# Optimization experiments

Measured on AMD Instinct MI355X. Metric: run time of the kernel, lower is better.

Reference implementation:

```python
import jax, jax.numpy as jnp
import numpy as np

# Config (matches init_kwargs)
B, S = 2, 2048            # 2 packed sequences of 2048 tokens (prefill)
HQ, HK, D = 32, 8, 128    # GQA: 32 query heads, 8 kv heads
G = HQ // HK              # group size 4
WINDOW = 1024             # sliding window
THETA = 10000.0


def setup_inputs() -> dict:
    key = jax.random.key(0)
    kq, kk, kv = jax.random.split(key, 3)
    n_tokens = B * S
    query = jax.random.normal(kq, (n_tokens, HQ * D), dtype=jnp.float32)
    key_t = jax.random.normal(kk, (n_tokens, HK * D), dtype=jnp.float32)
    value = jax.random.normal(kv, (n_tokens, HK * D), dtype=jnp.float32)
    # per-sequence positions restart at 0 for each packed sequence
    positions = jnp.tile(jnp.arange(S, dtype=jnp.int32), B)
    return {"query": query, "key": key_t, "value": value, "positions": positions}


def _rope(x, positions):
    # x: [B, S, H, D]; rotate-half (NeoX) RoPE
    half = D // 2
    inv_freq = 1.0 / (THETA ** (jnp.arange(0, half, dtype=jnp.float32) / half))
    ang = positions.astype(jnp.float32)[:, None] * inv_freq[None, :]   # [B*S, D/2]
    cos = jnp.cos(ang).reshape(B, S, 1, half)
    sin = jnp.sin(ang).reshape(B, S, 1, half)
    x1, x2 = x[..., :half], x[..., half:]
    return jnp.concatenate([x1 * cos - x2 * sin, x2 * cos + x1 * sin], axis=-1)


def reference(query, key, value, positions):
    q = query.reshape(B, S, HQ, D)
    k = key.reshape(B, S, HK, D)
    v = value.reshape(B, S, HK, D)
    q = _rope(q, positions)
    k = _rope(k, positions)
    # GQA: split q heads into [HK, G]
    qg = q.reshape(B, S, HK, G, D)
    scale = 1.0 / jnp.sqrt(jnp.float32(D))
    # scores: [B, HK, G, Sq, Skv]
    scores = jnp.einsum('bqhgd,bshd->bhgqs', qg, k) * scale
    i = jnp.arange(S)[:, None]
    j = jnp.arange(S)[None, :]
    # causal + sliding window: j <= i and i - j < WINDOW
    mask = (j <= i) & ((i - j) < WINDOW)
    scores = jnp.where(mask[None, None, None], scores, jnp.float32(-1e30))
    attn = jax.nn.softmax(scores, axis=-1)
    out = jnp.einsum('bhgqs,bshd->bqhgd', attn, v)   # [B, Sq, HK, G, D]
    return out.reshape(B * S, HQ * D)
```

## Files before the change

### kernel.cpp

```cpp
#include <hip/hip_runtime.h>
#include <stdint.h>

#define NB 2
#define NS 2048
#define NHK 8
#define ND 128
#define NWIN 1024

using bf16x8 = __bf16 __attribute__((ext_vector_type(8)));
using f32x4  = float  __attribute__((ext_vector_type(4)));
using f32x8  = float  __attribute__((ext_vector_type(8)));
using u16x8  = unsigned short __attribute__((ext_vector_type(8)));
using u32x4  = unsigned int   __attribute__((ext_vector_type(4)));

#define L2_10K (13.287712379549449f / 64.0f)
#define MASKV (-3.0e38f)

static __device__ __forceinline__ float ex2(float x) {
  return __builtin_amdgcn_exp2f(x);
}

static __device__ __forceinline__ unsigned short f2bf(float x) {
  unsigned int u = __builtin_bit_cast(unsigned int, x);
  u += 0x7FFFu + ((u >> 16) & 1u);
  return (unsigned short)(u >> 16);
}

static __device__ __forceinline__ unsigned int cvtpk(float lo, float hi) {
  unsigned int r;
  asm("v_cvt_pk_bf16_f32 %0, %1, %2" : "=v"(r) : "v"(lo), "v"(hi));
  return r;
}

static __device__ __forceinline__ void gll16(const void* g, void* l) {
  __builtin_amdgcn_global_load_lds(
      (const __attribute__((address_space(1))) void*)g,
      (__attribute__((address_space(3))) void*)l, 16, 0, 0);
}

#define ROR(x, N) __builtin_bit_cast(float, __builtin_amdgcn_mov_dpp( \
    __builtin_bit_cast(int, (x)), 0x120 + (N), 0xF, 0xF, false))

__global__ __launch_bounds__(64) void build_tab(float* __restrict__ tab) {
  const int p = blockIdx.x, f = threadIdx.x;
  float s, c;
  __sincosf((float)p * ex2(-(float)f * L2_10K), &s, &c);
  tab[(size_t)p * 128 + f] = c;
  tab[(size_t)p * 128 + 64 + f] = s;
}

__global__ __launch_bounds__(256) void prepass(
    const float* __restrict__ kin, const float* __restrict__ vin,
    const int* __restrict__ pos, const float* __restrict__ tab,
    unsigned short* __restrict__ kimg, unsigned int* __restrict__ vimg) {
  const int bid = blockIdx.x;
  const int ti = bid & 63, gidx = bid >> 6;
  const int hk = gidx & 7, b = gidx >> 3;
  const int t = threadIdx.x;

  unsigned short* kout = kimg + (size_t)bid * 4096;
#pragma unroll
  for (int uu = 0; uu < 2; ++uu) {
    const int u = t * 2 + uu;
    const int j = u >> 4;
    const int d0 = ((u & 15) << 3) ^ ((j & 7) << 3);
    const int tok = (b << 11) + (ti << 5) + j;
    const float* kp = kin + (size_t)tok * (NHK * ND) + hk * ND;
    f32x8 a = *(const f32x8*)(kp + d0);
    f32x8 p = *(const f32x8*)(kp + (d0 ^ 64));
    const float* tr = tab + (size_t)(pos[tok] & 2047) * 128 + (d0 & 63);
    f32x8 c8 = *(const f32x8*)tr;
    f32x8 s8 = *(const f32x8*)(tr + 64);
    u16x8 o;
#pragma unroll
    for (int i = 0; i < 8; ++i) {
      float val = (d0 < 64) ? (a[i] * c8[i] - p[i] * s8[i])
                            : (a[i] * c8[i] + p[i] * s8[i]);
      o[i] = f2bf(val);
    }
    *(u16x8*)(kout + (size_t)u * 8) = o;
  }

  unsigned int* vout = vimg + (size_t)bid * 2048;
  {
    const int d = t >> 1;
    const int jp0 = (t & 1) << 3;
    const float* vp = vin + (size_t)((b << 11) + (ti << 5)) * (NHK * ND) + hk * ND + d;
    unsigned int o[8];
#pragma unroll
    for (int i = 0; i < 8; ++i)
      o[i] = cvtpk(vp[(size_t)(jp0 + i) * (NHK * ND)],
                   vp[(size_t)(jp0 + i + 16) * (NHK * ND)]);
    u32x4 w0 = {o[0], o[1], o[2], o[3]};
    u32x4 w1 = {o[4], o[5], o[6], o[7]};
    *(u32x4*)(vout + d * 16 + jp0) = w0;
    *(u32x4*)(vout + d * 16 + jp0 + 4) = w1;
  }
}

template <bool PRE>
__global__ __launch_bounds__(256, 2) void attn_fwd(
    const float* __restrict__ qin, const float* __restrict__ kin,
    const float* __restrict__ vin, const int* __restrict__ pos,
    const char* __restrict__ kimg, const char* __restrict__ vimg,
    float* __restrict__ out) {
  __shared__ __align__(16) char Kb[2][8192];
  __shared__ __align__(16) char Vb[2][8192];
  __shared__ __align__(16) unsigned int Pw[4][32 * 20];

  const int B = blockIdx.x;
  const int group = (B & 7) + ((B >> 9) << 3);
  const int qt = 63 - ((B >> 3) & 63);
  const int hk = group & 7, b = group >> 3;

  const int tid = threadIdx.x;
  const int w = tid >> 6, lane = tid & 63, h = lane >> 4, ln = lane & 15;
  const int g = w;
  const int q0b = qt << 5;
  int lo = q0b - (NWIN - 1);
  if (lo < 0) lo = 0;
  lo &= ~31;
  const int ti0 = lo >> 5;
  const int nt = (q0b >> 5) - ti0 + 1;

  const size_t gbase = (size_t)group * 64 * 8192;
  const char* kg = PRE ? kimg + gbase + (size_t)(w * 128 + lane) * 16 : nullptr;
  const char* vg = PRE ? vimg + gbase + (size_t)(w * 128 + lane) * 16 : nullptr;

  auto stage = [&](int cur, int ti) {
    if constexpr (PRE) {
      const char* ks = kg + (size_t)ti * 8192;
      const char* vs = vg + (size_t)ti * 8192;
      char* kd = &Kb[cur][w * 2048];
      char* vd = &Vb[cur][w * 2048];
      gll16(ks, kd);
      gll16(ks + 1024, kd + 1024);
      gll16(vs, vd);
      gll16(vs + 1024, vd + 1024);
    } else {
      const int j = tid >> 3;
      const int du = (tid & 7) << 4;
      const int tok = (b << 11) + (ti << 5) + j;
      const float* kp = kin + (size_t)tok * (NHK * ND) + hk * ND;
      const float pj = (float)pos[tok];
#pragma unroll
      for (int gq = 0; gq < 2; ++gq) {
        const int dd = du + gq * 8;
        f32x8 a = *(const f32x8*)(kp + dd);
        f32x8 p = *(const f32x8*)(kp + (dd ^ 64));
        u16x8 o;
#pragma unroll
        for (int i = 0; i < 8; ++i) {
          float s, c;
          __sincosf(pj * ex2(-(float)((dd & 63) + i) * L2_10K), &s, &c);
          float val = (dd < 64) ? (a[i] * c - p[i] * s) : (a[i] * c + p[i] * s);
          o[i] = f2bf(val);
        }
        *(u16x8*)(&Kb[cur][((j << 8) + (dd << 1)) ^ ((j & 7) << 4)]) = o;
      }
      const int d = tid >> 1;
      const int jp0 = (tid & 1) << 3;
      const float* vp = vin + (size_t)((b << 11) + (ti << 5)) * (NHK * ND) + hk * ND + d;
      unsigned int o[8];
#pragma unroll
      for (int i = 0; i < 8; ++i)
        o[i] = cvtpk(vp[(size_t)(jp0 + i) * (NHK * ND)],
                     vp[(size_t)(jp0 + i + 16) * (NHK * ND)]);
      unsigned int* vb32 = (unsigned int*)Vb[cur];
      u32x4 w0 = {o[0], o[1], o[2], o[3]};
      u32x4 w1 = {o[4], o[5], o[6], o[7]};
      *(u32x4*)(vb32 + d * 16 + jp0) = w0;
      *(u32x4*)(vb32 + d * 16 + jp0 + 4) = w1;
    }
  };

  stage(0, ti0);

  const float QSC = 0.08838834764831845f * 1.4426950408889634f;
  bf16x8 qfr[2][4];
#pragma unroll
  for (int hf = 0; hf < 2; ++hf) {
    const int qrow = q0b + hf * 16 + ln;
    const size_t tokq = (size_t)(b << 11) + qrow;
    const float* qp = qin + tokq * 4096 + (hk * 4 + g) * 128;
    const float posq = (float)pos[tokq];
    const int r0 = h << 3;
    const int r1 = 32 + (h << 3);
    f32x8 a0 = *(const f32x8*)(qp + r0);
    f32x8 a1 = *(const f32x8*)(qp + r1);
    f32x8 a2 = *(const f32x8*)(qp + r0 + 64);
    f32x8 a3 = *(const f32x8*)(qp + r1 + 64);
    u16x8 u0, u1, u2, u3;
#pragma unroll
    for (int i = 0; i < 8; ++i) {
      float c0, s0, c1, s1;
      __sincosf(posq * ex2(-(float)(r0 + i) * L2_10K), &s0, &c0);
      __sincosf(posq * ex2(-(float)(r1 + i) * L2_10K), &s1, &c1);
      u0[i] = f2bf((a0[i] * c0 - a2[i] * s0) * QSC);
      u1[i] = f2bf((a1[i] * c1 - a3[i] * s1) * QSC);
      u2[i] = f2bf((a2[i] * c0 + a0[i] * s0) * QSC);
      u3[i] = f2bf((a3[i] * c1 + a1[i] * s1) * QSC);
    }
    qfr[hf][0] = __builtin_bit_cast(bf16x8, u0);
    qfr[hf][1] = __builtin_bit_cast(bf16x8, u1);
    qfr[hf][2] = __builtin_bit_cast(bf16x8, u2);
    qfr[hf][3] = __builtin_bit_cast(bf16x8, u3);
  }

  f32x4 Oc[2][8] = {};
  float m[2][4] = {{-1e30f, -1e30f, -1e30f, -1e30f},
                   {-1e30f, -1e30f, -1e30f, -1e30f}};
  float lsum[2][4] = {};
  unsigned int* pw = Pw[w];
  const int sw = (ln & 7) << 4;

  for (int t = 0; t < nt; ++t) {
    const int cur = t & 1;
    asm volatile("s_waitcnt vmcnt(0)" ::: "memory");
    __syncthreads();
    if (t + 1 < nt) stage(cur ^ 1, ti0 + t + 1);

    const int j0 = (ti0 + t) << 5;
    const char* KB = Kb[cur];

    f32x4 sS[2][2] = {};
    __builtin_amdgcn_s_setprio(1);
#pragma unroll
    for (int c = 0; c < 4; ++c) {
      const bf16x8 k0 = *(const bf16x8*)(
          KB + (((ln << 8) + (c << 6) + (h << 4)) ^ sw));
      const bf16x8 k1 = *(const bf16x8*)(
          KB + ((((16 + ln) << 8) + (c << 6) + (h << 4)) ^ sw));
      sS[0][0] = __builtin_amdgcn_mfma_f32_16x16x32_bf16(qfr[0][c], k0, sS[0][0], 0, 0, 0);
      sS[0][1] = __builtin_amdgcn_mfma_f32_16x16x32_bf16(qfr[0][c], k1, sS[0][1], 0, 0, 0);
      sS[1][0] = __builtin_amdgcn_mfma_f32_16x16x32_bf16(qfr[1][c], k0, sS[1][0], 0, 0, 0);
      sS[1][1] = __builtin_amdgcn_mfma_f32_16x16x32_bf16(qfr[1][c], k1, sS[1][1], 0, 0, 0);
    }
    __builtin_amdgcn_s_setprio(0);

    if ((j0 >= q0b) || (j0 < q0b - 992)) {
#pragma unroll
      for (int hf = 0; hf < 2; ++hf)
#pragma unroll
        for (int r = 0; r < 4; ++r) {
          const int irow = q0b + hf * 16 + (h << 2) + r;
          const int jc0 = j0 + ln, jc1 = jc0 + 16;
          if (!(jc0 <= irow && irow - jc0 < NWIN)) sS[hf][0][r] = MASKV;
          if (!(jc1 <= irow && irow - jc1 < NWIN)) sS[hf][1][r] = MASKV;
        }
    }

    float ov = MASKV;
    float tmax[2][4];
#pragma unroll
    for (int hf = 0; hf < 2; ++hf)
#pragma unroll
      for (int r = 0; r < 4; ++r) {
        tmax[hf][r] = fmaxf(sS[hf][0][r], sS[hf][1][r]);
        ov = fmaxf(ov, tmax[hf][r] - m[hf][r]);
      }
    if (__any(ov > 8.0f)) {
#pragma unroll
      for (int hf = 0; hf < 2; ++hf)
#pragma unroll
        for (int r = 0; r < 4; ++r) {
          float tm = tmax[hf][r];
          tm = fmaxf(tm, ROR(tm, 1));
          tm = fmaxf(tm, ROR(tm, 2));
          tm = fmaxf(tm, ROR(tm, 4));
          tm = fmaxf(tm, ROR(tm, 8));
          const float mn = fmaxf(m[hf][r], tm);
          const float co = ex2(m[hf][r] - mn);
          m[hf][r] = mn;
          lsum[hf][r] *= co;
#pragma unroll
          for (int db = 0; db < 8; ++db) Oc[hf][db][r] *= co;
        }
    }
#pragma unroll
    for (int hf = 0; hf < 2; ++hf)
#pragma unroll
      for (int r = 0; r < 4; ++r) {
        const float e0 = ex2(sS[hf][0][r] - m[hf][r]);
        const float e1 = ex2(sS[hf][1][r] - m[hf][r]);
        lsum[hf][r] += e0 + e1;
        pw[(hf * 16 + (h << 2) + r) * 20 + ln] = cvtpk(e0, e1);
      }

    asm volatile("s_waitcnt lgkmcnt(0)" ::: "memory");
    const bf16x8 pa0 = *(const bf16x8*)(pw + (ln * 20 + (h << 2)));
    const bf16x8 pa1 = *(const bf16x8*)(pw + ((16 + ln) * 20 + (h << 2)));
    const unsigned int* VB = (const unsigned int*)Vb[cur];
    __builtin_amdgcn_s_setprio(1);
#pragma unroll
    for (int db = 0; db < 8; ++db) {
      const bf16x8 vv = *(const bf16x8*)(VB + ((((db << 4) + ln) << 4) + (h << 2)));
      Oc[0][db] = __builtin_amdgcn_mfma_f32_16x16x32_bf16(pa0, vv, Oc[0][db], 0, 0, 0);
      Oc[1][db] = __builtin_amdgcn_mfma_f32_16x16x32_bf16(pa1, vv, Oc[1][db], 0, 0, 0);
    }
    __builtin_amdgcn_s_setprio(0);
  }

#pragma unroll
  for (int hf = 0; hf < 2; ++hf)
#pragma unroll
    for (int r = 0; r < 4; ++r) {
      float rs = lsum[hf][r];
      rs += ROR(rs, 1);
      rs += ROR(rs, 2);
      rs += ROR(rs, 4);
      rs += ROR(rs, 8);
      const float rl = 1.0f / rs;
      const int irow = q0b + hf * 16 + (h << 2) + r;
      float* op = out + ((size_t)(b << 11) + irow) * 4096 + (hk * 4 + g) * 128 + ln;
#pragma unroll
      for (int db = 0; db < 8; ++db) op[db * 16] = Oc[hf][db][r] * rl;
    }
}

extern "C" void kernel_launch(void* const* d_in, const int* in_sizes, int n_in,
                              void* d_out, int out_size, void* d_ws, size_t ws_size,
                              hipStream_t stream) {
  const float* q = (const float*)d_in[0];
  const float* k = (const float*)d_in[1];
  const float* v = (const float*)d_in[2];
  const int* pos = (const int*)d_in[3];
  float* out = (float*)d_out;

  const size_t TAB = (size_t)2048 * 128 * 4;
  const size_t KIMG = (size_t)16 * 64 * 8192;
  const size_t need = TAB + 2 * KIMG;

  if (ws_size >= need) {
    float* tab = (float*)d_ws;
    char* kimg = (char*)d_ws + TAB;
    char* vimg = kimg + KIMG;
    build_tab<<<2048, 64, 0, stream>>>(tab);
    prepass<<<1024, 256, 0, stream>>>(k, v, pos, tab,
                                      (unsigned short*)kimg, (unsigned int*)vimg);
    attn_fwd<true><<<1024, 256, 0, stream>>>(q, k, v, pos, kimg, vimg, out);
  } else {
    attn_fwd<false><<<1024, 256, 0, stream>>>(q, k, v, pos, nullptr, nullptr, out);
  }
}
```

Baseline: 112.4 us.

## Compute transposed scores so P feeds PV MFMA via permlane swaps, dropping LDS

Swaps the MFMA operands so the score tile comes out transposed (keys per lane-group, queries per lane). The softmax probabilities can then be repacked into the PV A-operand with v_permlane32/16_swap instead of a round trip through LDS. Row max and sum now need cross-lane shuffles. The V image layout changes to match the new operand layout, the per-wave P scratch buffer is removed, and occupancy hint rises to 3 blocks per CU. Risks: extra shuffles in the rescale path, and register pressure under the tighter launch bound.

```diff
diff --git a/kernel.cpp b/kernel.cpp
--- a/kernel.cpp
+++ b/kernel.cpp
@@ -9,6 +9,7 @@
 
 using bf16x8 = __bf16 __attribute__((ext_vector_type(8)));
 using f32x4  = float  __attribute__((ext_vector_type(4)));
+using f32x2  = float  __attribute__((ext_vector_type(2)));
 using f32x8  = float  __attribute__((ext_vector_type(8)));
 using u16x8  = unsigned short __attribute__((ext_vector_type(8)));
 using u32x4  = unsigned int   __attribute__((ext_vector_type(4)));
@@ -37,9 +38,6 @@
       (const __attribute__((address_space(1))) void*)g,
       (__attribute__((address_space(3))) void*)l, 16, 0, 0);
 }
-
-#define ROR(x, N) __builtin_bit_cast(float, __builtin_amdgcn_mov_dpp( \
-    __builtin_bit_cast(int, (x)), 0x120 + (N), 0xF, 0xF, false))
 
 __global__ __launch_bounds__(64) void build_tab(float* __restrict__ tab) {
   const int p = blockIdx.x, f = threadIdx.x;
@@ -52,7 +50,7 @@
 __global__ __launch_bounds__(256) void prepass(
     const float* __restrict__ kin, const float* __restrict__ vin,
     const int* __restrict__ pos, const float* __restrict__ tab,
-    unsigned short* __restrict__ kimg, unsigned int* __restrict__ vimg) {
+    unsigned short* __restrict__ kimg, unsigned short* __restrict__ vimg) {
   const int bid = blockIdx.x;
   const int ti = bid & 63, gidx = bid >> 6;
   const int hk = gidx & 7, b = gidx >> 3;
@@ -81,32 +79,33 @@
     *(u16x8*)(kout + (size_t)u * 8) = o;
   }
 
-  unsigned int* vout = vimg + (size_t)bid * 2048;
+  unsigned short* vout = vimg + (size_t)bid * 4096;
   {
-    const int d = t >> 1;
-    const int jp0 = (t & 1) << 3;
-    const float* vp = vin + (size_t)((b << 11) + (ti << 5)) * (NHK * ND) + hk * ND + d;
-    unsigned int o[8];
-#pragma unroll
-    for (int i = 0; i < 8; ++i)
-      o[i] = cvtpk(vp[(size_t)(jp0 + i) * (NHK * ND)],
-                   vp[(size_t)(jp0 + i + 16) * (NHK * ND)]);
-    u32x4 w0 = {o[0], o[1], o[2], o[3]};
-    u32x4 w1 = {o[4], o[5], o[6], o[7]};
-    *(u32x4*)(vout + d * 16 + jp0) = w0;
-    *(u32x4*)(vout + d * 16 + jp0 + 4) = w1;
+    const int d0 = (t >> 2) << 1;
+    const int kp4 = t & 3;
+    const int tok0 = (b << 11) + (ti << 5) + (kp4 << 3);
+    const float* vp = vin + (size_t)tok0 * (NHK * ND) + hk * ND + d0;
+    u16x8 lo, hi;
+#pragma unroll
+    for (int i = 0; i < 8; ++i) {
+      f32x2 r = *(const f32x2*)(vp + (size_t)i * (NHK * ND));
+      lo[i] = f2bf(r[0]);
+      hi[i] = f2bf(r[1]);
+    }
+    const int sub = kp4 ^ ((d0 >> 1) & 3);
+    *(u16x8*)(vout + d0 * 32 + sub * 8) = lo;
+    *(u16x8*)(vout + (d0 + 1) * 32 + sub * 8) = hi;
   }
 }
 
 template <bool PRE>
-__global__ __launch_bounds__(256, 2) void attn_fwd(
+__global__ __launch_bounds__(256, 3) void attn_fwd(
     const float* __restrict__ qin, const float* __restrict__ kin,
     const float* __restrict__ vin, const int* __restrict__ pos,
     const char* __restrict__ kimg, const char* __restrict__ vimg,
     float* __restrict__ out) {
   __shared__ __align__(16) char Kb[2][8192];
   __shared__ __align__(16) char Vb[2][8192];
-  __shared__ __align__(16) unsigned int Pw[4][32 * 20];
 
   const int B = blockIdx.x;
   const int group = (B & 7) + ((B >> 9) << 3);
@@ -158,19 +157,20 @@
         }
         *(u16x8*)(&Kb[cur][((j << 8) + (dd << 1)) ^ ((j & 7) << 4)]) = o;
       }
-      const int d = tid >> 1;
-      const int jp0 = (tid & 1) << 3;
-      const float* vp = vin + (size_t)((b << 11) + (ti << 5)) * (NHK * ND) + hk * ND + d;
-      unsigned int o[8];
-#pragma unroll
-      for (int i = 0; i < 8; ++i)
-        o[i] = cvtpk(vp[(size_t)(jp0 + i) * (NHK * ND)],
-                     vp[(size_t)(jp0 + i + 16) * (NHK * ND)]);
-      unsigned int* vb32 = (unsigned int*)Vb[cur];
-      u32x4 w0 = {o[0], o[1], o[2], o[3]};
-      u32x4 w1 = {o[4], o[5], o[6], o[7]};
-      *(u32x4*)(vb32 + d * 16 + jp0) = w0;
-      *(u32x4*)(vb32 + d * 16 + jp0 + 4) = w1;
+      const int d0 = (tid >> 2) << 1;
+      const int kp4 = tid & 3;
+      const float* vp = vin + (size_t)((b << 11) + (ti << 5) + (kp4 << 3)) * (NHK * ND) + hk * ND + d0;
+      u16x8 lov, hiv;
+#pragma unroll
+      for (int i = 0; i < 8; ++i) {
+        f32x2 r = *(const f32x2*)(vp + (size_t)i * (NHK * ND));
+        lov[i] = f2bf(r[0]);
+        hiv[i] = f2bf(r[1]);
+      }
+      const int sub = kp4 ^ ((d0 >> 1) & 3);
+      unsigned short* vb16 = (unsigned short*)Vb[cur];
+      *(u16x8*)(vb16 + d0 * 32 + sub * 8) = lov;
+      *(u16x8*)(vb16 + (d0 + 1) * 32 + sub * 8) = hiv;
     }
   };
 
@@ -208,11 +208,10 @@
   }
 
   f32x4 Oc[2][8] = {};
-  float m[2][4] = {{-1e30f, -1e30f, -1e30f, -1e30f},
-                   {-1e30f, -1e30f, -1e30f, -1e30f}};
-  float lsum[2][4] = {};
-  unsigned int* pw = Pw[w];
+  float msh[2] = {-1e30f, -1e30f};
+  float lsum[2] = {};
   const int sw = (ln & 7) << 4;
+  const int vsub = (h ^ ((ln >> 1) & 3)) << 4;
 
   for (int t = 0; t < nt; ++t) {
     const int cur = t & 1;
@@ -223,7 +222,7 @@
     const int j0 = (ti0 + t) << 5;
     const char* KB = Kb[cur];
 
-    f32x4 sS[2][2] = {};
+    f32x4 sT[2][2] = {};
     __builtin_amdgcn_s_setprio(1);
 #pragma unroll
     for (int c = 0; c < 4; ++c) {
@@ -231,91 +230,102 @@
           KB + (((ln << 8) + (c << 6) + (h << 4)) ^ sw));
       const bf16x8 k1 = *(const bf16x8*)(
           KB + ((((16 + ln) << 8) + (c << 6) + (h << 4)) ^ sw));
-      sS[0][0] = __builtin_amdgcn_mfma_f32_16x16x32_bf16(qfr[0][c], k0, sS[0][0], 0, 0, 0);
-      sS[0][1] = __builtin_amdgcn_mfma_f32_16x16x32_bf16(qfr[0][c], k1, sS[0][1], 0, 0, 0);
-      sS[1][0] = __builtin_amdgcn_mfma_f32_16x16x32_bf16(qfr[1][c], k0, sS[1][0], 0, 0, 0);
-      sS[1][1] = __builtin_amdgcn_mfma_f32_16x16x32_bf16(qfr[1][c], k1, sS[1][1], 0, 0, 0);
+      sT[0][0] = __builtin_amdgcn_mfma_f32_16x16x32_bf16(k0, qfr[0][c], sT[0][0], 0, 0, 0);
+      sT[0][1] = __builtin_amdgcn_mfma_f32_16x16x32_bf16(k1, qfr[0][c], sT[0][1], 0, 0, 0);
+      sT[1][0] = __builtin_amdgcn_mfma_f32_16x16x32_bf16(k0, qfr[1][c], sT[1][0], 0, 0, 0);
+      sT[1][1] = __builtin_amdgcn_mfma_f32_16x16x32_bf16(k1, qfr[1][c], sT[1][1], 0, 0, 0);
     }
     __builtin_amdgcn_s_setprio(0);
 
     if ((j0 >= q0b) || (j0 < q0b - 992)) {
 #pragma unroll
-      for (int hf = 0; hf < 2; ++hf)
-#pragma unroll
-        for (int r = 0; r < 4; ++r) {
-          const int irow = q0b + hf * 16 + (h << 2) + r;
-          const int jc0 = j0 + ln, jc1 = jc0 + 16;
-          if (!(jc0 <= irow && irow - jc0 < NWIN)) sS[hf][0][r] = MASKV;
-          if (!(jc1 <= irow && irow - jc1 < NWIN)) sS[hf][1][r] = MASKV;
-        }
-    }
-
-    float ov = MASKV;
-    float tmax[2][4];
-#pragma unroll
-    for (int hf = 0; hf < 2; ++hf)
-#pragma unroll
-      for (int r = 0; r < 4; ++r) {
-        tmax[hf][r] = fmaxf(sS[hf][0][r], sS[hf][1][r]);
-        ov = fmaxf(ov, tmax[hf][r] - m[hf][r]);
+      for (int qh = 0; qh < 2; ++qh) {
+        const int irow = q0b + qh * 16 + ln;
+#pragma unroll
+        for (int ki = 0; ki < 2; ++ki)
+#pragma unroll
+          for (int r = 0; r < 4; ++r) {
+            const int j = j0 + ki * 16 + (h << 2) + r;
+            if (!(j <= irow && irow - j < NWIN)) sT[qh][ki][r] = MASKV;
+          }
       }
+    }
+
+    float pm[2];
+#pragma unroll
+    for (int qh = 0; qh < 2; ++qh) {
+      const f32x4 s0 = sT[qh][0], s1 = sT[qh][1];
+      pm[qh] = fmaxf(fmaxf(fmaxf(s0[0], s0[1]), fmaxf(s0[2], s0[3])),
+                     fmaxf(fmaxf(s1[0], s1[1]), fmaxf(s1[2], s1[3])));
+    }
+    const float ov = fmaxf(pm[0] - msh[0], pm[1] - msh[1]);
     if (__any(ov > 8.0f)) {
 #pragma unroll
-      for (int hf = 0; hf < 2; ++hf)
-#pragma unroll
-        for (int r = 0; r < 4; ++r) {
-          float tm = tmax[hf][r];
-          tm = fmaxf(tm, ROR(tm, 1));
-          tm = fmaxf(tm, ROR(tm, 2));
-          tm = fmaxf(tm, ROR(tm, 4));
-          tm = fmaxf(tm, ROR(tm, 8));
-          const float mn = fmaxf(m[hf][r], tm);
-          const float co = ex2(m[hf][r] - mn);
-          m[hf][r] = mn;
-          lsum[hf][r] *= co;
-#pragma unroll
-          for (int db = 0; db < 8; ++db) Oc[hf][db][r] *= co;
-        }
-    }
-#pragma unroll
-    for (int hf = 0; hf < 2; ++hf)
-#pragma unroll
-      for (int r = 0; r < 4; ++r) {
-        const float e0 = ex2(sS[hf][0][r] - m[hf][r]);
-        const float e1 = ex2(sS[hf][1][r] - m[hf][r]);
-        lsum[hf][r] += e0 + e1;
-        pw[(hf * 16 + (h << 2) + r) * 20 + ln] = cvtpk(e0, e1);
+      for (int qh = 0; qh < 2; ++qh) {
+        float M = pm[qh];
+        M = fmaxf(M, __shfl_xor(M, 16));
+        M = fmaxf(M, __shfl_xor(M, 32));
+        const float mn = fmaxf(msh[qh], M);
+        const float co = ex2(msh[qh] - mn);
+        msh[qh] = mn;
+        lsum[qh] *= co;
+        float coO[4];
+#pragma unroll
+        for (int r = 0; r < 4; ++r) coO[r] = __shfl(co, (h << 2) + r);
+#pragma unroll
+        for (int db = 0; db < 8; ++db)
+#pragma unroll
+          for (int r = 0; r < 4; ++r) Oc[qh][db][r] *= coO[r];
       }
-
-    asm volatile("s_waitcnt lgkmcnt(0)" ::: "memory");
-    const bf16x8 pa0 = *(const bf16x8*)(pw + (ln * 20 + (h << 2)));
-    const bf16x8 pa1 = *(const bf16x8*)(pw + ((16 + ln) * 20 + (h << 2)));
-    const unsigned int* VB = (const unsigned int*)Vb[cur];
+    }
+
+    bf16x8 pa[2];
+#pragma unroll
+    for (int qh = 0; qh < 2; ++qh) {
+      float e[2][4];
+#pragma unroll
+      for (int ki = 0; ki < 2; ++ki)
+#pragma unroll
+        for (int r = 0; r < 4; ++r) e[ki][r] = ex2(sT[qh][ki][r] - msh[qh]);
+      lsum[qh] += ((e[0][0] + e[0][1]) + (e[0][2] + e[0][3])) +
+                  ((e[1][0] + e[1][1]) + (e[1][2] + e[1][3]));
+      unsigned int A = cvtpk(e[0][0], e[0][1]);
+      unsigned int Bk = cvtpk(e[0][2], e[0][3]);
+      unsigned int C = cvtpk(e[1][0], e[1][1]);
+      unsigned int D = cvtpk(e[1][2], e[1][3]);
+      asm volatile("v_permlane32_swap_b32 %0, %1" : "+v"(A), "+v"(C));
+      asm volatile("v_permlane16_swap_b32 %0, %1" : "+v"(A), "+v"(C));
+      asm volatile("v_permlane32_swap_b32 %0, %1" : "+v"(Bk), "+v"(D));
+      asm volatile("v_permlane16_swap_b32 %0, %1" : "+v"(Bk), "+v"(D));
+      u32x4 pk4 = {A, Bk, C, D};
+      pa[qh] = __builtin_bit_cast(bf16x8, pk4);
+    }
+
+    const char* VB = Vb[cur];
     __builtin_amdgcn_s_setprio(1);
 #pragma unroll
     for (int db = 0; db < 8; ++db) {
-      const bf16x8 vv = *(const bf16x8*)(VB + ((((db << 4) + ln) << 4) + (h << 2)));
-      Oc[0][db] = __builtin_amdgcn_mfma_f32_16x16x32_bf16(pa0, vv, Oc[0][db], 0, 0, 0);
-      Oc[1][db] = __builtin_amdgcn_mfma_f32_16x16x32_bf16(pa1, vv, Oc[1][db], 0, 0, 0);
+      const bf16x8 vv = *(const bf16x8*)(VB + (db << 10) + (ln << 6) + vsub);
+      Oc[0][db] = __builtin_amdgcn_mfma_f32_16x16x32_bf16(pa[0], vv, Oc[0][db], 0, 0, 0);
+      Oc[1][db] = __builtin_amdgcn_mfma_f32_16x16x32_bf16(pa[1], vv, Oc[1][db], 0, 0, 0);
     }
     __builtin_amdgcn_s_setprio(0);
   }
 
 #pragma unroll
-  for (int hf = 0; hf < 2; ++hf)
+  for (int qh = 0; qh < 2; ++qh) {
+    float ls = lsum[qh];
+    ls += __shfl_xor(ls, 16);
+    ls += __shfl_xor(ls, 32);
 #pragma unroll
     for (int r = 0; r < 4; ++r) {
-      float rs = lsum[hf][r];
-      rs += ROR(rs, 1);
-      rs += ROR(rs, 2);
-      rs += ROR(rs, 4);
-      rs += ROR(rs, 8);
-      const float rl = 1.0f / rs;
-      const int irow = q0b + hf * 16 + (h << 2) + r;
+      const float rl = 1.0f / __shfl(ls, (h << 2) + r);
+      const int irow = q0b + qh * 16 + (h << 2) + r;
       float* op = out + ((size_t)(b << 11) + irow) * 4096 + (hk * 4 + g) * 128 + ln;
 #pragma unroll
-      for (int db = 0; db < 8; ++db) op[db * 16] = Oc[hf][db][r] * rl;
-    }
+      for (int db = 0; db < 8; ++db) op[db * 16] = Oc[qh][db][r] * rl;
+    }
+  }
 }
 
 extern "C" void kernel_launch(void* const* d_in, const int* in_sizes, int n_in,
@@ -337,7 +347,7 @@
     char* vimg = kimg + KIMG;
     build_tab<<<2048, 64, 0, stream>>>(tab);
     prepass<<<1024, 256, 0, stream>>>(k, v, pos, tab,
-                                      (unsigned short*)kimg, (unsigned int*)vimg);
+                                      (unsigned short*)kimg, (unsigned short*)vimg);
     attn_fwd<true><<<1024, 256, 0, stream>>>(q, k, v, pos, kimg, vimg, out);
   } else {
     attn_fwd<false><<<1024, 256, 0, stream>>>(q, k, v, pos, nullptr, nullptr, out);
```

After: 94.15 us. 1.19x faster.
